# Kernel optimization log

Hardware: AMD Instinct MI355X
Metric: run time of the kernel (lower is better)

## Reference

```python
import jax, jax.numpy as jnp
import numpy as np


def setup_inputs() -> dict:
    key = jax.random.key(0)
    k1, k2, k3 = jax.random.split(key, 3)
    x = jax.random.normal(k1, (8, 64, 256, 256), dtype=jnp.float32)
    weight = jax.random.normal(k2, (64, 64, 3, 3), dtype=jnp.float32)
    bias = jax.random.normal(k3, (64,), dtype=jnp.float32)
    return {"x": x, "weight": weight, "bias": bias}


def _fft_conv_nd(x, weight, bias):
    # x: [B, Cin, *spatial]; weight: [Cout, Cin, *kernel]
    ndim = x.ndim - 2
    spatial = x.shape[2:]
    kernel = weight.shape[2:]
    conv_sizes = tuple(s + k - 1 for s, k in zip(spatial, kernel))
    valid_sizes = tuple(s - k + 1 for s, k in zip(spatial, kernel))

    # flip kernel over spatial dims (module flips before the FFT)
    w_flipped = jnp.flip(weight, axis=tuple(range(2, 2 + ndim)))

    # zero-pad at the end of each spatial dim to the full-conv size
    x_pad = jnp.pad(x, [(0, 0), (0, 0)] + [(0, c - s) for s, c in zip(spatial, conv_sizes)])
    w_pad = jnp.pad(w_flipped, [(0, 0), (0, 0)] + [(0, c - k) for k, c in zip(kernel, conv_sizes)])

    axes = tuple(range(-ndim, 0))
    x_fft = jnp.fft.fftn(x_pad, axes=axes)
    w_fft = jnp.fft.fftn(w_pad, axes=axes)
    # channel mixing per frequency bin
    conv_fft = jnp.einsum('bi...,oi...->bo...', x_fft, w_fft)
    conv = jnp.fft.ifftn(conv_fft, axes=axes).real.astype(x.dtype)

    # extract the 'valid' region starting at k-1 in each spatial dim
    slices = (slice(None), slice(None)) + tuple(
        slice(k - 1, k - 1 + v) for k, v in zip(kernel, valid_sizes))
    out = conv[slices]
    return out + bias.reshape((1, -1) + (1,) * ndim)


def reference(x, weight, bias):
    return _fft_conv_nd(x, weight, bias)
```

## Files before the change

kernel.cpp:

```cpp
#include <hip/hip_runtime.h>
#include <cstdint>

typedef float  f32x4  __attribute__((ext_vector_type(4)));
typedef float  f32x16 __attribute__((ext_vector_type(16)));
typedef short  s16x8  __attribute__((ext_vector_type(8)));

__device__ __forceinline__ unsigned short f2bf(float f){
  unsigned int u = __float_as_uint(f);
  return (unsigned short)((u + 0x7FFFu + ((u >> 16) & 1u)) >> 16);
}

__device__ alignas(16) unsigned short g_Wt[9*64*64];

__global__ void wt_kernel(const float* __restrict__ w){
  int t = blockIdx.x*256 + threadIdx.x;
  if (t >= 9*64*64) return;
  int ci = t & 63, o = (t >> 6) & 63, tap = t >> 12;
  int kh = tap/3, kw = tap%3;
  g_Wt[t] = f2bf(w[((o*64 + ci)*3 + kh)*3 + kw]);
}

#define SLAB 8448

__global__ __launch_bounds__(256, 2) void conv_main(const float* __restrict__ x,
                                                    const float* __restrict__ bias,
                                                    float* __restrict__ out){
  __shared__ alignas(16) char smem[4*SLAB];
  const int quarter = blockIdx.x;
  const int ystrip  = blockIdx.y;
  const int b       = blockIdx.z;
  const int n0 = quarter*64, y0 = ystrip*8;
  const int tid = threadIdx.x, lane = tid & 63, wv = tid >> 6;
  const int wr = wv >> 1, wc = wv & 1;
  const float* xb = x + (size_t)b*64*65536;

  s16x8 aw[36];
  {
    const int o = wr*32 + (lane & 31);
    const int cib = (lane >> 5) * 8;
    #pragma unroll
    for (int tap = 0; tap < 9; ++tap)
      #pragma unroll
      for (int part = 0; part < 4; ++part)
        aw[tap*4+part] = *reinterpret_cast<const s16x8*>(
            &g_Wt[(tap*64 + o)*64 + part*16 + cib]);
  }

  const int ob = wr*32 + 4*(lane >> 5);
  float bv[16];
  #pragma unroll
  for (int reg = 0; reg < 16; ++reg)
    bv[reg] = bias[ob + (reg & 3) + 8*(reg >> 2)];

  #pragma unroll
  for (int r = 0; r < 3; ++r){
    const int rr = y0 + r;
    char* slab = smem + r*SLAB;
    #pragma unroll
    for (int it = 0; it < 3; ++it){
      int tau = it*256 + tid;
      if (tau < 544){
        int cp = tau & 31, q = tau >> 5, c0 = q*4;
        int cg = n0 + c0; if (cg > 252) cg = 252;
        const float* p = xb + (size_t)(2*cp)*65536 + rr*256 + cg;
        float4 v0 = *reinterpret_cast<const float4*>(p);
        float4 v1 = *reinterpret_cast<const float4*>(p + 65536);
        const float* a0 = reinterpret_cast<const float*>(&v0);
        const float* a1 = reinterpret_cast<const float*>(&v1);
        #pragma unroll
        for (int j = 0; j < 4; ++j){
          int c = c0 + j;
          if (c < 66){
            unsigned int pk = (unsigned)f2bf(a0[j]) | ((unsigned)f2bf(a1[j]) << 16);
            *reinterpret_cast<unsigned int*>(slab + ((c*128 + cp*4) ^ ((c & 7) << 4))) = pk;
          }
        }
      }
    }
  }
  __syncthreads();

  for (int yloc = 0; yloc < 8; ++yloc){
    const int y = y0 + yloc;

    float4 p0[3], p1[3];
    if (yloc < 7){
      int rr = y + 3; if (rr > 255) rr = 255;
      #pragma unroll
      for (int it = 0; it < 3; ++it){
        int tau = it*256 + tid;
        if (tau < 544){
          int cp = tau & 31, q = tau >> 5;
          int cg = n0 + q*4; if (cg > 252) cg = 252;
          const float* p = xb + (size_t)(2*cp)*65536 + rr*256 + cg;
          p0[it] = *reinterpret_cast<const float4*>(p);
          p1[it] = *reinterpret_cast<const float4*>(p + 65536);
        }
      }
    }

    if (y < 254){
      f32x16 acc;
      #pragma unroll
      for (int i = 0; i < 16; ++i) acc[i] = 0.f;

      #pragma unroll
      for (int kh = 0; kh < 3; ++kh){
        const char* slab = smem + ((yloc + kh) & 3)*SLAB;
        #pragma unroll
        for (int kw = 0; kw < 3; ++kw){
          const int col = wc*32 + (lane & 31) + kw;
          const int swz = (col & 7) << 4;
          const int cb  = col*128 + ((lane >> 5) << 4);
          #pragma unroll
          for (int part = 0; part < 4; ++part){
            s16x8 bf = *reinterpret_cast<const s16x8*>(
                slab + ((cb + part*32) ^ swz));
            acc = __builtin_amdgcn_mfma_f32_32x32x16_bf16(aw[(kh*3+kw)*4 + part], bf, acc, 0, 0, 0);
          }
        }
      }

      const int nl = n0 + wc*32 + (lane & 31);
      if (nl < 254){
        size_t rowbase = (((size_t)b*64 + ob)*254 + y)*254 + nl;
        #pragma unroll
        for (int reg = 0; reg < 16; ++reg){
          int od = (reg & 3) + 8*(reg >> 2);
          out[rowbase + (size_t)od*64516] = acc[reg] + bv[reg];
        }
      }
    }

    if (yloc < 7){
      char* slab = smem + ((yloc + 3) & 3)*SLAB;
      #pragma unroll
      for (int it = 0; it < 3; ++it){
        int tau = it*256 + tid;
        if (tau < 544){
          int cp = tau & 31, q = tau >> 5, c0 = q*4;
          const float* a0 = reinterpret_cast<const float*>(&p0[it]);
          const float* a1 = reinterpret_cast<const float*>(&p1[it]);
          #pragma unroll
          for (int j = 0; j < 4; ++j){
            int c = c0 + j;
            if (c < 66){
              unsigned int pk = (unsigned)f2bf(a0[j]) | ((unsigned)f2bf(a1[j]) << 16);
              *reinterpret_cast<unsigned int*>(slab + ((c*128 + cp*4) ^ ((c & 7) << 4))) = pk;
            }
          }
        }
      }
    }
    __syncthreads();
  }
}

extern "C" void kernel_launch(void* const* d_in, const int* in_sizes, int n_in,
                              void* d_out, int out_size, void* d_ws, size_t ws_size,
                              hipStream_t stream) {
  const float* x    = (const float*)d_in[0];
  const float* wgt  = (const float*)d_in[1];
  const float* bias = (const float*)d_in[2];
  float* out = (float*)d_out;

  wt_kernel<<<144, 256, 0, stream>>>(wgt);
  conv_main<<<dim3(4, 32, 8), 256, 0, stream>>>(x, bias, out);
}
```

Before: 92.85 us.

## Compute two output rows per iteration with double-row shared slabs

Each block now covers 16 output rows instead of 8 and computes two rows per loop iteration, using three double-row bf16 slabs in shared memory with a wider swizzle. This reduces redundant global reads of halo rows and halves the number of barriers per output row. In exchange it doubles the accumulator registers alongside the resident weight fragments, which risks occupancy loss, and it halves the grid size.

```diff
diff --git a/kernel.cpp b/kernel.cpp
--- a/kernel.cpp
+++ b/kernel.cpp
@@ -1,7 +1,6 @@
 #include <hip/hip_runtime.h>
 #include <cstdint>
 
-typedef float  f32x4  __attribute__((ext_vector_type(4)));
 typedef float  f32x16 __attribute__((ext_vector_type(16)));
 typedef short  s16x8  __attribute__((ext_vector_type(8)));
 
@@ -20,16 +19,15 @@
   g_Wt[t] = f2bf(w[((o*64 + ci)*3 + kh)*3 + kw]);
 }
 
-#define SLAB 8448
+#define DSLAB 16896
 
 __global__ __launch_bounds__(256, 2) void conv_main(const float* __restrict__ x,
                                                     const float* __restrict__ bias,
                                                     float* __restrict__ out){
-  __shared__ alignas(16) char smem[4*SLAB];
-  const int quarter = blockIdx.x;
-  const int ystrip  = blockIdx.y;
-  const int b       = blockIdx.z;
-  const int n0 = quarter*64, y0 = ystrip*8;
+  __shared__ alignas(16) char smem[3*DSLAB];
+  const int n0 = blockIdx.x*64, y0 = blockIdx.y*16, b = blockIdx.z;
+  const int rows  = min(16, 254 - y0);
+  const int niter = rows >> 1;
   const int tid = threadIdx.x, lane = tid & 63, wv = tid >> 6;
   const int wr = wv >> 1, wc = wv & 1;
   const float* xb = x + (size_t)b*64*65536;
@@ -53,9 +51,8 @@
     bv[reg] = bias[ob + (reg & 3) + 8*(reg >> 2)];
 
   #pragma unroll
-  for (int r = 0; r < 3; ++r){
-    const int rr = y0 + r;
-    char* slab = smem + r*SLAB;
+  for (int d = 0; d < 2; ++d){
+    const int rr = y0 + 2*d;
     #pragma unroll
     for (int it = 0; it < 3; ++it){
       int tau = it*256 + tid;
@@ -63,16 +60,22 @@
         int cp = tau & 31, q = tau >> 5, c0 = q*4;
         int cg = n0 + c0; if (cg > 252) cg = 252;
         const float* p = xb + (size_t)(2*cp)*65536 + rr*256 + cg;
-        float4 v0 = *reinterpret_cast<const float4*>(p);
-        float4 v1 = *reinterpret_cast<const float4*>(p + 65536);
-        const float* a0 = reinterpret_cast<const float*>(&v0);
-        const float* a1 = reinterpret_cast<const float*>(&v1);
+        float4 v00 = *reinterpret_cast<const float4*>(p);
+        float4 v01 = *reinterpret_cast<const float4*>(p + 65536);
+        float4 v10 = *reinterpret_cast<const float4*>(p + 256);
+        float4 v11 = *reinterpret_cast<const float4*>(p + 65536 + 256);
+        const float* a00 = (const float*)&v00; const float* a01 = (const float*)&v01;
+        const float* a10 = (const float*)&v10; const float* a11 = (const float*)&v11;
         #pragma unroll
         for (int j = 0; j < 4; ++j){
           int c = c0 + j;
           if (c < 66){
-            unsigned int pk = (unsigned)f2bf(a0[j]) | ((unsigned)f2bf(a1[j]) << 16);
-            *reinterpret_cast<unsigned int*>(slab + ((c*128 + cp*4) ^ ((c & 7) << 4))) = pk;
+            unsigned pk0 = (unsigned)f2bf(a00[j]) | ((unsigned)f2bf(a01[j]) << 16);
+            unsigned pk1 = (unsigned)f2bf(a10[j]) | ((unsigned)f2bf(a11[j]) << 16);
+            int swz = (c & 15) << 4;
+            int base = c*256 + cp*4;
+            *(unsigned*)(smem + d*DSLAB + ((base      ) ^ swz)) = pk0;
+            *(unsigned*)(smem + d*DSLAB + ((base + 128) ^ swz)) = pk1;
           }
         }
       }
@@ -80,12 +83,16 @@
   }
   __syncthreads();
 
-  for (int yloc = 0; yloc < 8; ++yloc){
-    const int y = y0 + yloc;
+  int d0 = 0;
+  for (int t = 0; t < niter; ++t){
+    const int y = y0 + 2*t;
+    const int d1 = (d0 + 1 > 2) ? 0 : d0 + 1;
+    const int d2 = 3 - d0 - d1;
 
-    float4 p0[3], p1[3];
-    if (yloc < 7){
-      int rr = y + 3; if (rr > 255) rr = 255;
+    float4 pf[3][4];
+    const bool hav = (t + 1 < niter);
+    if (hav){
+      const int rr = y + 4;
       #pragma unroll
       for (int it = 0; it < 3; ++it){
         int tau = it*256 + tid;
@@ -93,66 +100,84 @@
           int cp = tau & 31, q = tau >> 5;
           int cg = n0 + q*4; if (cg > 252) cg = 252;
           const float* p = xb + (size_t)(2*cp)*65536 + rr*256 + cg;
-          p0[it] = *reinterpret_cast<const float4*>(p);
-          p1[it] = *reinterpret_cast<const float4*>(p + 65536);
+          pf[it][0] = *reinterpret_cast<const float4*>(p);
+          pf[it][1] = *reinterpret_cast<const float4*>(p + 65536);
+          pf[it][2] = *reinterpret_cast<const float4*>(p + 256);
+          pf[it][3] = *reinterpret_cast<const float4*>(p + 65536 + 256);
         }
       }
     }
 
-    if (y < 254){
-      f32x16 acc;
+    f32x16 acc[2];
+    #pragma unroll
+    for (int r = 0; r < 2; ++r)
       #pragma unroll
-      for (int i = 0; i < 16; ++i) acc[i] = 0.f;
+      for (int i = 0; i < 16; ++i) acc[r][i] = 0.f;
 
+    #pragma unroll
+    for (int kh = 0; kh < 3; ++kh){
       #pragma unroll
-      for (int kh = 0; kh < 3; ++kh){
-        const char* slab = smem + ((yloc + kh) & 3)*SLAB;
+      for (int row = 0; row < 2; ++row){
+        const int lrr = kh + row;
+        const int dd = (lrr >> 1) ? d1 : d0;
+        const int pp = lrr & 1;
+        const char* slab = smem + dd*DSLAB;
         #pragma unroll
         for (int kw = 0; kw < 3; ++kw){
-          const int col = wc*32 + (lane & 31) + kw;
-          const int swz = (col & 7) << 4;
-          const int cb  = col*128 + ((lane >> 5) << 4);
+          const int c = wc*32 + (lane & 31) + kw;
+          const int swz = (c & 15) << 4;
+          const int cb = c*256 + pp*128 + ((lane >> 5) << 4);
           #pragma unroll
           for (int part = 0; part < 4; ++part){
             s16x8 bf = *reinterpret_cast<const s16x8*>(
                 slab + ((cb + part*32) ^ swz));
-            acc = __builtin_amdgcn_mfma_f32_32x32x16_bf16(aw[(kh*3+kw)*4 + part], bf, acc, 0, 0, 0);
+            acc[row] = __builtin_amdgcn_mfma_f32_32x32x16_bf16(
+                aw[(kh*3+kw)*4 + part], bf, acc[row], 0, 0, 0);
           }
-        }
-      }
-
-      const int nl = n0 + wc*32 + (lane & 31);
-      if (nl < 254){
-        size_t rowbase = (((size_t)b*64 + ob)*254 + y)*254 + nl;
-        #pragma unroll
-        for (int reg = 0; reg < 16; ++reg){
-          int od = (reg & 3) + 8*(reg >> 2);
-          out[rowbase + (size_t)od*64516] = acc[reg] + bv[reg];
         }
       }
     }
 
-    if (yloc < 7){
-      char* slab = smem + ((yloc + 3) & 3)*SLAB;
+    const int nl = n0 + wc*32 + (lane & 31);
+    if (nl < 254){
+      #pragma unroll
+      for (int row = 0; row < 2; ++row){
+        size_t rowbase = (((size_t)b*64 + ob)*254 + (y + row))*254 + nl;
+        #pragma unroll
+        for (int reg = 0; reg < 16; ++reg){
+          int od = (reg & 3) + 8*(reg >> 2);
+          out[rowbase + (size_t)od*64516] = acc[row][reg] + bv[reg];
+        }
+      }
+    }
+
+    if (hav){
       #pragma unroll
       for (int it = 0; it < 3; ++it){
         int tau = it*256 + tid;
         if (tau < 544){
           int cp = tau & 31, q = tau >> 5, c0 = q*4;
-          const float* a0 = reinterpret_cast<const float*>(&p0[it]);
-          const float* a1 = reinterpret_cast<const float*>(&p1[it]);
+          const float* a00 = (const float*)&pf[it][0];
+          const float* a01 = (const float*)&pf[it][1];
+          const float* a10 = (const float*)&pf[it][2];
+          const float* a11 = (const float*)&pf[it][3];
           #pragma unroll
           for (int j = 0; j < 4; ++j){
             int c = c0 + j;
             if (c < 66){
-              unsigned int pk = (unsigned)f2bf(a0[j]) | ((unsigned)f2bf(a1[j]) << 16);
-              *reinterpret_cast<unsigned int*>(slab + ((c*128 + cp*4) ^ ((c & 7) << 4))) = pk;
+              unsigned pk0 = (unsigned)f2bf(a00[j]) | ((unsigned)f2bf(a01[j]) << 16);
+              unsigned pk1 = (unsigned)f2bf(a10[j]) | ((unsigned)f2bf(a11[j]) << 16);
+              int swz = (c & 15) << 4;
+              int base = c*256 + cp*4;
+              *(unsigned*)(smem + d2*DSLAB + ((base      ) ^ swz)) = pk0;
+              *(unsigned*)(smem + d2*DSLAB + ((base + 128) ^ swz)) = pk1;
             }
           }
         }
       }
     }
     __syncthreads();
+    d0 = d1;
   }
 }
 
@@ -165,5 +190,5 @@
   float* out = (float*)d_out;
 
   wt_kernel<<<144, 256, 0, stream>>>(wgt);
-  conv_main<<<dim3(4, 32, 8), 256, 0, stream>>>(x, bias, out);
+  conv_main<<<dim3(4, 16, 8), 256, 0, stream>>>(x, bias, out);
 }
```

Result: slower. 163.5 us (+76.1%).
